# Kernel optimization log

Measured on AMD Instinct MI355X. Metric: run time of the kernel, lower is better.

The kernel has to match this reference:

```python
import jax, jax.numpy as jnp
import numpy as np


def setup_inputs() -> dict:
    key = jax.random.key(0)
    k_h, k_w1, k_w2 = jax.random.split(key, 3)
    B, S, D = 8, 2048, 1024
    H = 2 * D  # reasoning_net hidden width
    # xavier_uniform-style scaled weights
    lim1 = float(np.sqrt(6.0 / (D + H)))
    lim2 = float(np.sqrt(6.0 / (H + D)))
    return {
        "hidden_states": jax.random.normal(k_h, (B, S, D), dtype=jnp.float32),
        "W1": jax.random.uniform(k_w1, (D, H), dtype=jnp.float32, minval=-lim1, maxval=lim1),
        "b1": jnp.zeros((H,), dtype=jnp.float32),
        "W2": jax.random.uniform(k_w2, (H, D), dtype=jnp.float32, minval=-lim2, maxval=lim2),
        "b2": jnp.zeros((D,), dtype=jnp.float32),
    }


def reference(hidden_states, W1, b1, W2, b2):
    """Chain reasoning forward.

    The torch loop carries output[:, -1:], but reasoning_net is a per-token MLP
    (Linear over the last dim), so processed[:, -1:] == MLP(current token) and the
    carried state never influences appended outputs. Faithful closed form:
      out[:, 0]  = hidden_states[:, 0]
      out[:, i]  = MLP(hidden_states[:, i])  for i >= 1
    Dropout is identity (eval). GELU is exact (torch default).
    """
    rest = hidden_states[:, 1:, :]  # [B, S-1, D]
    h = jax.nn.gelu(jnp.einsum("bsd,dh->bsh", rest, W1) + b1, approximate=False)
    out_rest = jnp.einsum("bsh,hd->bsd", h, W2) + b2
    return jnp.concatenate([hidden_states[:, :1, :], out_rest], axis=1)
```

## Files before the change

### kernel.cpp

```cpp
#include <hip/hip_runtime.h>
#include <hip/hip_bf16.h>
#include <cstdint>
#include <cstddef>

typedef unsigned short u16;
typedef __attribute__((ext_vector_type(8))) __bf16 bf16x8;
typedef __attribute__((ext_vector_type(8))) unsigned short u16x8;
typedef __attribute__((ext_vector_type(4))) float f32x4;

__device__ __forceinline__ void gload_lds16(const void* g, void* l) {
    __builtin_amdgcn_global_load_lds(
        (const __attribute__((address_space(1))) unsigned int*)g,
        (__attribute__((address_space(3))) unsigned int*)l,
        16, 0, 0);
}

__device__ __forceinline__ u16 f2bf(float f) {
    union { float f; unsigned int u; } v; v.f = f;
    unsigned int r = v.u + 0x7fffu + ((v.u >> 16) & 1u);
    return (u16)(r >> 16);
}

__device__ __forceinline__ float gelu_tanh(float x) {
    const float z = 0.7978845608028654f * x * (1.0f + 0.044715f * x * x);
    const float t = __builtin_amdgcn_exp2f(2.885390081777927f * z);
    const float th = 1.0f - 2.0f * __builtin_amdgcn_rcpf(t + 1.0f);
    return 0.5f * x * (1.0f + th);
}

template <int GELU, int OUT_BF16>
__global__ void gemm_bt(const u16* __restrict__ A,
                        const u16* __restrict__ Bt,
                        const float* __restrict__ bias,
                        void* __restrict__ Cv,
                        int M, int N, int K) {
    __shared__ __align__(16) char smem[16896];
    u16* As = (u16*)smem;
    u16* Bs = (u16*)(smem + 8192);
    float* Ct = (float*)smem;

    const int tid  = threadIdx.x;
    const int lane = tid & 63;
    const int wave = tid >> 6;
    const int wm   = (wave >> 1) * 64;
    const int wn   = (wave & 1) * 64;
    const int mrow = lane & 15;
    const int half = lane >> 4;

    const size_t ldb = (size_t)K * 2;
    const char* Ab = (const char*)(A + (size_t)blockIdx.x * 128 * K);
    const char* Bb = (const char*)(Bt + (size_t)blockIdx.y * 128 * K);

    const int r0 = tid >> 2, g0 = tid & 3;
    const int r1 = r0 + 64;
    const size_t soff0 = (size_t)r0 * ldb + (size_t)((g0 ^ ((r0 >> 1) & 3)) << 4);
    const size_t soff1 = (size_t)r1 * ldb + (size_t)((g0 ^ ((r1 >> 1) & 3)) << 4);

    int alds[4], blds[4];
#pragma unroll
    for (int t = 0; t < 4; ++t) {
        const int ra = wm + t * 16 + mrow;
        alds[t] = ra * 64 + ((half ^ ((ra >> 1) & 3)) << 4);
        const int rb = wn + t * 16 + mrow;
        blds[t] = rb * 64 + ((half ^ ((rb >> 1) & 3)) << 4);
    }

    f32x4 acc[4][4];
#pragma unroll
    for (int i = 0; i < 4; ++i)
#pragma unroll
        for (int j = 0; j < 4; ++j) acc[i][j] = f32x4{0.f, 0.f, 0.f, 0.f};

    for (int k0 = 0; k0 < K; k0 += 32) {
        const size_t kb = (size_t)k0 * 2;
        gload_lds16(Ab + soff0 + kb, (char*)As + tid * 16);
        gload_lds16(Ab + soff1 + kb, (char*)As + (tid + 256) * 16);
        gload_lds16(Bb + soff0 + kb, (char*)Bs + tid * 16);
        gload_lds16(Bb + soff1 + kb, (char*)Bs + (tid + 256) * 16);
        __syncthreads();

        bf16x8 af[4], bfr[4];
#pragma unroll
        for (int t = 0; t < 4; ++t) {
            af[t]  = *(const bf16x8*)((const char*)As + alds[t]);
            bfr[t] = *(const bf16x8*)((const char*)Bs + blds[t]);
        }

#pragma unroll
        for (int mi = 0; mi < 4; ++mi)
#pragma unroll
            for (int ni = 0; ni < 4; ++ni)
                acc[mi][ni] = __builtin_amdgcn_mfma_f32_16x16x32_bf16(
                    af[mi], bfr[ni], acc[mi][ni], 0, 0, 0);

        __syncthreads();
    }

    const int lrow0 = wm + half * 4;
    const int lcol0 = wn + mrow;
    const int growbase = blockIdx.x * 128;
    const int gcolbase = blockIdx.y * 128;
    const int rr_rd = tid >> 3, cs_rd = (tid & 7) * 16;

#pragma unroll
    for (int c = 0; c < 4; ++c) {
        __syncthreads();
        if ((wm >> 6) == (c >> 1)) {
            const int mi0 = (c & 1) * 2;
#pragma unroll
            for (int dmi = 0; dmi < 2; ++dmi) {
                const int mi = mi0 + dmi;
#pragma unroll
                for (int ni = 0; ni < 4; ++ni) {
                    const int col = lcol0 + ni * 16;
                    const float bv = bias[gcolbase + col];
#pragma unroll
                    for (int r = 0; r < 4; ++r) {
                        const int rr = (mi * 16 + lrow0 + r) & 31;
                        float v = acc[mi][ni][r] + bv;
                        if (GELU) v = gelu_tanh(v);
                        Ct[rr * 132 + col] = v;
                    }
                }
            }
        }
        __syncthreads();
        const float* ct = &Ct[rr_rd * 132 + cs_rd];
        const f32x4 v0 = *(const f32x4*)(ct);
        const f32x4 v1 = *(const f32x4*)(ct + 4);
        const f32x4 v2 = *(const f32x4*)(ct + 8);
        const f32x4 v3 = *(const f32x4*)(ct + 12);
        const int grow = growbase + 32 * c + rr_rd;
        if (OUT_BF16) {
            u16x8 lo, hi;
#pragma unroll
            for (int j = 0; j < 4; ++j) {
                lo[j] = f2bf(v0[j]); lo[j + 4] = f2bf(v1[j]);
                hi[j] = f2bf(v2[j]); hi[j + 4] = f2bf(v3[j]);
            }
            u16* p = (u16*)Cv + (size_t)grow * N + gcolbase + cs_rd;
            *(u16x8*)(p)     = lo;
            *(u16x8*)(p + 8) = hi;
        } else {
            float* p = (float*)Cv + (size_t)grow * N + gcolbase + cs_rd;
            *(f32x4*)(p)      = v0;
            *(f32x4*)(p + 4)  = v1;
            *(f32x4*)(p + 8)  = v2;
            *(f32x4*)(p + 12) = v3;
        }
    }
}

__global__ void transpose_cvt_bf16(const float* __restrict__ src,
                                   u16* __restrict__ dst, int R, int C) {
    __shared__ u16 t[32][33];
    const int bx = blockIdx.x * 32;
    const int by = blockIdx.y * 32;
    const int x = threadIdx.x, y = threadIdx.y;
    for (int i = 0; i < 32; i += 8)
        t[y + i][x] = f2bf(src[(size_t)(by + y + i) * C + (bx + x)]);
    __syncthreads();
    for (int i = 0; i < 32; i += 8)
        dst[(size_t)(bx + y + i) * R + (by + x)] = t[x][y + i];
}

__global__ void cvt_bf16(const float* __restrict__ src, u16* __restrict__ dst,
                         long long n) {
    const long long i = ((long long)blockIdx.x * blockDim.x + threadIdx.x) * 4;
    if (i + 3 < n) {
        const float4 v = *(const float4*)(src + i);
        ushort4 o;
        o.x = f2bf(v.x); o.y = f2bf(v.y); o.z = f2bf(v.z); o.w = f2bf(v.w);
        *(ushort4*)(dst + i) = o;
    }
}

__global__ void fixup_first_token(const float* __restrict__ hs,
                                  float* __restrict__ out, int S, int D) {
    const size_t base = (size_t)blockIdx.x * S * D;
    for (int i = threadIdx.x; i < D; i += blockDim.x)
        out[base + i] = hs[base + i];
}

extern "C" void kernel_launch(void* const* d_in, const int* in_sizes, int n_in,
                              void* d_out, int out_size, void* d_ws, size_t ws_size,
                              hipStream_t stream) {
    const float* X  = (const float*)d_in[0];
    const float* W1 = (const float*)d_in[1];
    const float* b1 = (const float*)d_in[2];
    const float* W2 = (const float*)d_in[3];
    const float* b2 = (const float*)d_in[4];
    float* out = (float*)d_out;

    const int B = 8, S = 2048, D = 1024, H = 2048;
    const int M = B * S;

    u16* W1T = (u16*)d_ws;
    u16* W2T = W1T + (size_t)H * D;
    u16* Xb  = W2T + (size_t)D * H;
    const size_t wfixed = (size_t)H * D * 2 * 2;
    const size_t perrow = (size_t)(D + H) * 2;
    size_t avail_rows = (ws_size > wfixed) ? (ws_size - wfixed) / perrow : 0;
    int CM = (int)((avail_rows / 128) * 128);
    if (CM > M) CM = M;
    if (CM < 128) CM = 128;
    u16* Hb = Xb + (size_t)CM * D;

    dim3 tb(32, 8);
    transpose_cvt_bf16<<<dim3(H / 32, D / 32), tb, 0, stream>>>(W1, W1T, D, H);
    transpose_cvt_bf16<<<dim3(D / 32, H / 32), tb, 0, stream>>>(W2, W2T, H, D);

    for (int m0 = 0; m0 < M; m0 += CM) {
        const int rows = (M - m0 < CM) ? (M - m0) : CM;
        const long long n = (long long)rows * D;
        cvt_bf16<<<dim3((unsigned)(n / 1024)), dim3(256), 0, stream>>>(
            X + (size_t)m0 * D, Xb, n);
        dim3 g1(rows / 128, H / 128);
        gemm_bt<1, 1><<<g1, dim3(256), 0, stream>>>(
            Xb, W1T, b1, Hb, rows, H, D);
        dim3 g2(rows / 128, D / 128);
        gemm_bt<0, 0><<<g2, dim3(256), 0, stream>>>(
            Hb, W2T, b2, out + (size_t)m0 * D, rows, D, H);
    }

    fixup_first_token<<<dim3(B), dim3(256), 0, stream>>>(X, out, S, D);
}
```

Before: 327.9 us.

## Deepen GEMM K-tile to 64 and fuse preprocessing into one prep kernel

```diff
diff --git a/kernel.cpp b/kernel.cpp
--- a/kernel.cpp
+++ b/kernel.cpp
@@ -28,15 +28,15 @@
     return 0.5f * x * (1.0f + th);
 }
 
-template <int GELU, int OUT_BF16>
+template <int GELU, int OUT_BF16, int SKIP_S>
 __global__ void gemm_bt(const u16* __restrict__ A,
                         const u16* __restrict__ Bt,
                         const float* __restrict__ bias,
                         void* __restrict__ Cv,
-                        int M, int N, int K) {
-    __shared__ __align__(16) char smem[16896];
+                        int M, int N, int K, int row0) {
+    __shared__ __align__(16) char smem[32768];
     u16* As = (u16*)smem;
-    u16* Bs = (u16*)(smem + 8192);
+    u16* Bs = (u16*)(smem + 16384);
     float* Ct = (float*)smem;
 
     const int tid  = threadIdx.x;
@@ -51,19 +51,26 @@
     const char* Ab = (const char*)(A + (size_t)blockIdx.x * 128 * K);
     const char* Bb = (const char*)(Bt + (size_t)blockIdx.y * 128 * K);
 
-    const int r0 = tid >> 2, g0 = tid & 3;
-    const int r1 = r0 + 64;
-    const size_t soff0 = (size_t)r0 * ldb + (size_t)((g0 ^ ((r0 >> 1) & 3)) << 4);
-    const size_t soff1 = (size_t)r1 * ldb + (size_t)((g0 ^ ((r1 >> 1) & 3)) << 4);
-
-    int alds[4], blds[4];
-#pragma unroll
-    for (int t = 0; t < 4; ++t) {
-        const int ra = wm + t * 16 + mrow;
-        alds[t] = ra * 64 + ((half ^ ((ra >> 1) & 3)) << 4);
-        const int rb = wn + t * 16 + mrow;
-        blds[t] = rb * 64 + ((half ^ ((rb >> 1) & 3)) << 4);
-    }
+    size_t goff[4];
+    int loff[4];
+#pragma unroll
+    for (int i = 0; i < 4; ++i) {
+        const int L = tid + 256 * i, r = L >> 3, s = L & 7;
+        goff[i] = (size_t)r * ldb + (size_t)((s ^ (r & 7)) << 4);
+        loff[i] = L << 4;
+    }
+
+    int alds[2][4], blds[2][4];
+#pragma unroll
+    for (int j = 0; j < 2; ++j)
+#pragma unroll
+        for (int t = 0; t < 4; ++t) {
+            const int g = j * 4 + half;
+            const int ra = wm + t * 16 + mrow;
+            alds[j][t] = ra * 128 + ((g ^ (ra & 7)) << 4);
+            const int rb = wn + t * 16 + mrow;
+            blds[j][t] = rb * 128 + ((g ^ (rb & 7)) << 4);
+        }
 
     f32x4 acc[4][4];
 #pragma unroll
@@ -71,28 +78,31 @@
 #pragma unroll
         for (int j = 0; j < 4; ++j) acc[i][j] = f32x4{0.f, 0.f, 0.f, 0.f};
 
-    for (int k0 = 0; k0 < K; k0 += 32) {
+    for (int k0 = 0; k0 < K; k0 += 64) {
         const size_t kb = (size_t)k0 * 2;
-        gload_lds16(Ab + soff0 + kb, (char*)As + tid * 16);
-        gload_lds16(Ab + soff1 + kb, (char*)As + (tid + 256) * 16);
-        gload_lds16(Bb + soff0 + kb, (char*)Bs + tid * 16);
-        gload_lds16(Bb + soff1 + kb, (char*)Bs + (tid + 256) * 16);
-        __syncthreads();
-
-        bf16x8 af[4], bfr[4];
-#pragma unroll
-        for (int t = 0; t < 4; ++t) {
-            af[t]  = *(const bf16x8*)((const char*)As + alds[t]);
-            bfr[t] = *(const bf16x8*)((const char*)Bs + blds[t]);
-        }
-
-#pragma unroll
-        for (int mi = 0; mi < 4; ++mi)
-#pragma unroll
-            for (int ni = 0; ni < 4; ++ni)
-                acc[mi][ni] = __builtin_amdgcn_mfma_f32_16x16x32_bf16(
-                    af[mi], bfr[ni], acc[mi][ni], 0, 0, 0);
-
+#pragma unroll
+        for (int i = 0; i < 4; ++i)
+            gload_lds16(Ab + goff[i] + kb, (char*)As + loff[i]);
+#pragma unroll
+        for (int i = 0; i < 4; ++i)
+            gload_lds16(Bb + goff[i] + kb, (char*)Bs + loff[i]);
+        __syncthreads();
+
+#pragma unroll
+        for (int j = 0; j < 2; ++j) {
+            bf16x8 af[4], bfr[4];
+#pragma unroll
+            for (int t = 0; t < 4; ++t) {
+                af[t]  = *(const bf16x8*)((const char*)As + alds[j][t]);
+                bfr[t] = *(const bf16x8*)((const char*)Bs + blds[j][t]);
+            }
+#pragma unroll
+            for (int mi = 0; mi < 4; ++mi)
+#pragma unroll
+                for (int ni = 0; ni < 4; ++ni)
+                    acc[mi][ni] = __builtin_amdgcn_mfma_f32_16x16x32_bf16(
+                        af[mi], bfr[ni], acc[mi][ni], 0, 0, 0);
+        }
         __syncthreads();
     }
 
@@ -125,38 +135,39 @@
             }
         }
         __syncthreads();
-        const float* ct = &Ct[rr_rd * 132 + cs_rd];
-        const f32x4 v0 = *(const f32x4*)(ct);
-        const f32x4 v1 = *(const f32x4*)(ct + 4);
-        const f32x4 v2 = *(const f32x4*)(ct + 8);
-        const f32x4 v3 = *(const f32x4*)(ct + 12);
         const int grow = growbase + 32 * c + rr_rd;
-        if (OUT_BF16) {
-            u16x8 lo, hi;
-#pragma unroll
-            for (int j = 0; j < 4; ++j) {
-                lo[j] = f2bf(v0[j]); lo[j + 4] = f2bf(v1[j]);
-                hi[j] = f2bf(v2[j]); hi[j + 4] = f2bf(v3[j]);
+        const bool skip = SKIP_S && (((row0 + grow) & 2047) == 0);
+        if (!skip) {
+            const float* ct = &Ct[rr_rd * 132 + cs_rd];
+            const f32x4 v0 = *(const f32x4*)(ct);
+            const f32x4 v1 = *(const f32x4*)(ct + 4);
+            const f32x4 v2 = *(const f32x4*)(ct + 8);
+            const f32x4 v3 = *(const f32x4*)(ct + 12);
+            if (OUT_BF16) {
+                u16x8 lo, hi;
+#pragma unroll
+                for (int j = 0; j < 4; ++j) {
+                    lo[j] = f2bf(v0[j]); lo[j + 4] = f2bf(v1[j]);
+                    hi[j] = f2bf(v2[j]); hi[j + 4] = f2bf(v3[j]);
+                }
+                u16* p = (u16*)Cv + (size_t)grow * N + gcolbase + cs_rd;
+                *(u16x8*)(p)     = lo;
+                *(u16x8*)(p + 8) = hi;
+            } else {
+                float* p = (float*)Cv + (size_t)grow * N + gcolbase + cs_rd;
+                *(f32x4*)(p)      = v0;
+                *(f32x4*)(p + 4)  = v1;
+                *(f32x4*)(p + 8)  = v2;
+                *(f32x4*)(p + 12) = v3;
             }
-            u16* p = (u16*)Cv + (size_t)grow * N + gcolbase + cs_rd;
-            *(u16x8*)(p)     = lo;
-            *(u16x8*)(p + 8) = hi;
-        } else {
-            float* p = (float*)Cv + (size_t)grow * N + gcolbase + cs_rd;
-            *(f32x4*)(p)      = v0;
-            *(f32x4*)(p + 4)  = v1;
-            *(f32x4*)(p + 8)  = v2;
-            *(f32x4*)(p + 12) = v3;
-        }
-    }
-}
-
-__global__ void transpose_cvt_bf16(const float* __restrict__ src,
-                                   u16* __restrict__ dst, int R, int C) {
-    __shared__ u16 t[32][33];
-    const int bx = blockIdx.x * 32;
-    const int by = blockIdx.y * 32;
-    const int x = threadIdx.x, y = threadIdx.y;
+        }
+    }
+}
+
+__device__ __forceinline__ void tcvt_block(const float* __restrict__ src,
+                                           u16* __restrict__ dst, int R, int C,
+                                           int bx, int by, int x, int y,
+                                           u16 (*t)[33]) {
     for (int i = 0; i < 32; i += 8)
         t[y + i][x] = f2bf(src[(size_t)(by + y + i) * C + (bx + x)]);
     __syncthreads();
@@ -164,22 +175,31 @@
         dst[(size_t)(bx + y + i) * R + (by + x)] = t[x][y + i];
 }
 
-__global__ void cvt_bf16(const float* __restrict__ src, u16* __restrict__ dst,
-                         long long n) {
-    const long long i = ((long long)blockIdx.x * blockDim.x + threadIdx.x) * 4;
-    if (i + 3 < n) {
-        const float4 v = *(const float4*)(src + i);
-        ushort4 o;
-        o.x = f2bf(v.x); o.y = f2bf(v.y); o.z = f2bf(v.z); o.w = f2bf(v.w);
-        *(ushort4*)(dst + i) = o;
-    }
-}
-
-__global__ void fixup_first_token(const float* __restrict__ hs,
-                                  float* __restrict__ out, int S, int D) {
-    const size_t base = (size_t)blockIdx.x * S * D;
-    for (int i = threadIdx.x; i < D; i += blockDim.x)
-        out[base + i] = hs[base + i];
+__global__ void prep(const float* __restrict__ X, const float* __restrict__ W1,
+                     const float* __restrict__ W2, u16* __restrict__ Xb,
+                     u16* __restrict__ W1T, u16* __restrict__ W2T,
+                     float* __restrict__ out, long long nX) {
+    __shared__ u16 t[32][33];
+    const int b = blockIdx.x, tid = threadIdx.x;
+    const int x = tid & 31, y = tid >> 5;
+    if (b < 2048) {
+        tcvt_block(W1, W1T, 1024, 2048, (b & 63) * 32, (b >> 6) * 32, x, y, t);
+    } else if (b < 4096) {
+        const int bi = b - 2048;
+        tcvt_block(W2, W2T, 2048, 1024, (bi & 31) * 32, (bi >> 5) * 32, x, y, t);
+    } else if (b < 4104) {
+        const size_t base = (size_t)(b - 4096) * 2048 * 1024;
+        *(float4*)(out + base + tid * 4) = *(const float4*)(X + base + tid * 4);
+    } else {
+        const long long stride = (long long)4096 * 256 * 4;
+        for (long long i = ((long long)(b - 4104) * 256 + tid) * 4; i < nX;
+             i += stride) {
+            const float4 v = *(const float4*)(X + i);
+            ushort4 o;
+            o.x = f2bf(v.x); o.y = f2bf(v.y); o.z = f2bf(v.z); o.w = f2bf(v.w);
+            *(ushort4*)(Xb + i) = o;
+        }
+    }
 }
 
 extern "C" void kernel_launch(void* const* d_in, const int* in_sizes, int n_in,
@@ -198,30 +218,23 @@
     u16* W1T = (u16*)d_ws;
     u16* W2T = W1T + (size_t)H * D;
     u16* Xb  = W2T + (size_t)D * H;
-    const size_t wfixed = (size_t)H * D * 2 * 2;
-    const size_t perrow = (size_t)(D + H) * 2;
-    size_t avail_rows = (ws_size > wfixed) ? (ws_size - wfixed) / perrow : 0;
+    u16* Hb  = Xb + (size_t)M * D;
+    const size_t wfixed = (size_t)H * D * 2 * 2 + (size_t)M * D * 2;
+    size_t avail_rows = (ws_size > wfixed) ? (ws_size - wfixed) / ((size_t)H * 2) : 0;
     int CM = (int)((avail_rows / 128) * 128);
     if (CM > M) CM = M;
     if (CM < 128) CM = 128;
-    u16* Hb = Xb + (size_t)CM * D;
-
-    dim3 tb(32, 8);
-    transpose_cvt_bf16<<<dim3(H / 32, D / 32), tb, 0, stream>>>(W1, W1T, D, H);
-    transpose_cvt_bf16<<<dim3(D / 32, H / 32), tb, 0, stream>>>(W2, W2T, H, D);
+
+    prep<<<dim3(8200), dim3(256), 0, stream>>>(
+        X, W1, W2, Xb, W1T, W2T, out, (long long)M * D);
 
     for (int m0 = 0; m0 < M; m0 += CM) {
         const int rows = (M - m0 < CM) ? (M - m0) : CM;
-        const long long n = (long long)rows * D;
-        cvt_bf16<<<dim3((unsigned)(n / 1024)), dim3(256), 0, stream>>>(
-            X + (size_t)m0 * D, Xb, n);
         dim3 g1(rows / 128, H / 128);
-        gemm_bt<1, 1><<<g1, dim3(256), 0, stream>>>(
-            Xb, W1T, b1, Hb, rows, H, D);
+        gemm_bt<1, 1, 0><<<g1, dim3(256), 0, stream>>>(
+            Xb + (size_t)m0 * D, W1T, b1, Hb, rows, H, D, m0);
         dim3 g2(rows / 128, D / 128);
-        gemm_bt<0, 0><<<g2, dim3(256), 0, stream>>>(
-            Hb, W2T, b2, out + (size_t)m0 * D, rows, D, H);
-    }
-
-    fixup_first_token<<<dim3(B), dim3(256), 0, stream>>>(X, out, S, D);
-}
+        gemm_bt<0, 0, 1><<<g2, dim3(256), 0, stream>>>(
+            Hb, W2T, b2, out + (size_t)m0 * D, rows, D, H, m0);
+    }
+}
```

Measured after the change: 297.4 us. -9.3%, faster.
